# Performance work log

Hardware: AMD Instinct MI355X
Metric: run time of the kernel (lower is better)

The kernel has to match this reference:

```python
import jax, jax.numpy as jnp
import numpy as np
from math import sqrt

D_MODEL = 1024
B, T = 4, 4096


def setup_inputs() -> dict:
    key = jax.random.key(0)
    kx, kqk, kvo = jax.random.split(key, 3)
    x = jax.random.normal(kx, (B, T, D_MODEL), dtype=jnp.float32)
    # xavier_uniform for square [D, D]: limit = sqrt(6 / (D + D))
    limit = sqrt(6.0 / (2 * D_MODEL))
    QK = jax.random.uniform(kqk, (D_MODEL, D_MODEL), minval=-limit, maxval=limit, dtype=jnp.float32)
    VO = jax.random.uniform(kvo, (D_MODEL, D_MODEL), minval=-limit, maxval=limit, dtype=jnp.float32)
    return {"x": x, "QK": QK, "VO": VO}


def reference(x, QK, VO):
    d_model = QK.shape[0]
    # scores[b,t,u] = x[b,t,:] @ QK @ x[b,u,:]  -- precompute xQK once
    xQK = jnp.einsum('btd,de->bte', x, QK)                 # [B,T,D]
    scores = jnp.einsum('bte,bue->btu', xQK, x) / sqrt(d_model)  # [B,T,T]
    attn = jax.nn.softmax(scores, axis=2)
    # out[b,t,e] = attn @ x @ VO
    av = jnp.einsum('btu,bud->btd', attn, x)               # [B,T,D]
    return jnp.einsum('btd,de->bte', av, VO)
```

## Files before the change

### kernel.cpp

```cpp
#include <hip/hip_runtime.h>
#include <hip/hip_bf16.h>


#define BB 4
#define TT 4096
#define DD 1024

typedef __attribute__((ext_vector_type(8))) short bf16x8;
typedef __attribute__((ext_vector_type(4))) float f32x4;

__device__ __forceinline__ void gll16(const void* g, void* l) {
  __builtin_amdgcn_global_load_lds(
      (__attribute__((address_space(1))) void*)g,
      (__attribute__((address_space(3))) void*)l, 16, 0, 0);
}

#define WAIT_VM(n) asm volatile("s_waitcnt vmcnt(" #n ")" ::: "memory")
#define WAIT_LGKM0 do { asm volatile("s_waitcnt lgkmcnt(0)" ::: "memory"); \
                        __builtin_amdgcn_sched_barrier(0); } while (0)
#define BARRIER    do { __builtin_amdgcn_s_barrier(); \
                        __builtin_amdgcn_sched_barrier(0); } while (0)

__global__ __launch_bounds__(256) void xprep_k(const float* __restrict__ in,
                                               __hip_bfloat16* __restrict__ rm,
                                               __hip_bfloat16* __restrict__ cm,
                                               int R, int C, long bs) {
  in += (long)blockIdx.z * bs; rm += (long)blockIdx.z * bs; cm += (long)blockIdx.z * bs;
  __shared__ __hip_bfloat16 tile[64][65];
  int c0 = blockIdx.x * 64, r0 = blockIdx.y * 64;
  int tx = threadIdx.x & 63, ty = threadIdx.x >> 6;
#pragma unroll
  for (int i = 0; i < 16; ++i) {
    int r = ty + i * 4;
    __hip_bfloat16 v = __float2bfloat16(in[(long)(r0 + r) * C + c0 + tx]);
    tile[r][tx] = v;
    rm[(long)(r0 + r) * C + c0 + tx] = v;
  }
  __syncthreads();
#pragma unroll
  for (int i = 0; i < 16; ++i) {
    int c = ty + i * 4;
    cm[(long)(c0 + c) * R + r0 + tx] = tile[tx][c];
  }
}

__global__ __launch_bounds__(256) void transpose_cast_k(const float* __restrict__ in,
                                                        __hip_bfloat16* __restrict__ out,
                                                        int R, int C) {
  __shared__ __hip_bfloat16 tile[64][65];
  int c0 = blockIdx.x * 64, r0 = blockIdx.y * 64;
  int tx = threadIdx.x & 63, ty = threadIdx.x >> 6;
#pragma unroll
  for (int i = 0; i < 16; ++i) {
    int r = ty + i * 4;
    tile[r][tx] = __float2bfloat16(in[(long)(r0 + r) * C + c0 + tx]);
  }
  __syncthreads();
#pragma unroll
  for (int i = 0; i < 16; ++i) {
    int c = ty + i * 4;
    out[(long)(c0 + c) * R + r0 + tx] = tile[tx][c];
  }
}

__global__ __launch_bounds__(256) void zero_f32_k(float* __restrict__ p, int n) {
  int i = blockIdx.x * 256 + threadIdx.x;
  if (i < n) p[i] = 0.f;
}

template <typename OUT_T, int EPI>
__global__ __launch_bounds__(512, 2) void gemm256(
    const __hip_bfloat16* __restrict__ A,
    const __hip_bfloat16* __restrict__ Bt,
    OUT_T* __restrict__ C,
    int M, int N, int K, float alpha,
    long sAz, long sBz, long sCz, float* __restrict__ lsum) {
  __shared__ alignas(16) char smem[131072];
  A  += (long)blockIdx.z * sAz;
  Bt += (long)blockIdx.z * sBz;
  C  += (long)blockIdx.z * sCz;

  const int nwg = gridDim.x * gridDim.y;
  const int lin = blockIdx.x + gridDim.x * blockIdx.y;
  const int swz = (lin & 7) * (nwg >> 3) + (lin >> 3);
  const int gxsh = __popc(gridDim.x - 1);
  const int bx = swz & (gridDim.x - 1);
  const int by = swz >> gxsh;

  const int tid  = threadIdx.x;
  const int lane = tid & 63;
  const int wid  = tid >> 6;
  const int wr   = wid >> 2;
  const int wc   = wid & 3;
  const long m0 = (long)bx * 256;
  const long n0 = (long)by * 256;
  const int NT = K >> 6;

  const int srow = tid >> 3;
  const int sswz = (tid & 7) ^ (srow & 7);
  const __hip_bfloat16* gA = A  + (m0 + srow) * (long)K + sswz * 8;
  const __hip_bfloat16* gB = Bt + (n0 + srow) * (long)K + sswz * 8;

#define STG_A(s, c, D) gll16(gA + (long)(c) * 64 * K + (long)(s) * 64, \
                             smem + (D) + (c) * 8192 + wid * 1024)
#define STG_B(s, c, D) gll16(gB + (long)(c) * 64 * K + (long)(s) * 64, \
                             smem + (D) + 32768 + (c) * 8192 + wid * 1024)

  const int fr = lane & 15, l4 = lane >> 4, f7 = lane & 7;
  const char* a00 = smem +         (wr * 128 + fr) * 128 + ((l4    ) ^ f7) * 16;
  const char* a01 = smem +         (wr * 128 + fr) * 128 + ((4 | l4) ^ f7) * 16;
  const char* b00 = smem + 32768 + (wc * 64  + fr) * 128 + ((l4    ) ^ f7) * 16;
  const char* b01 = smem + 32768 + (wc * 64  + fr) * 128 + ((4 | l4) ^ f7) * 16;
  const char* a10 = a00 + 65536; const char* a11 = a01 + 65536;
  const char* b10 = b00 + 65536; const char* b11 = b01 + 65536;

  bf16x8 aq[4][2], bq[4][2];
#define RD_A(p0, p1, MIOFF)                                         \
  _Pragma("unroll") for (int mi_ = 0; mi_ < 4; ++mi_) {             \
    aq[mi_][0] = *(const bf16x8*)((p0) + ((MIOFF) + mi_) * 2048);   \
    aq[mi_][1] = *(const bf16x8*)((p1) + ((MIOFF) + mi_) * 2048);   \
  }
#define RD_B(p0, p1, NI0)                                           \
  _Pragma("unroll") for (int ni_ = 0; ni_ < 2; ++ni_) {             \
    bq[(NI0) + ni_][0] = *(const bf16x8*)((p0) + ((NI0) + ni_) * 2048); \
    bq[(NI0) + ni_][1] = *(const bf16x8*)((p1) + ((NI0) + ni_) * 2048); \
  }

  f32x4 acc[8][4];
#pragma unroll
  for (int mi = 0; mi < 8; ++mi)
#pragma unroll
    for (int ni = 0; ni < 4; ++ni)
      acc[mi][ni] = (f32x4){0.f, 0.f, 0.f, 0.f};

#define MFMA16(MI0, NI0)                                                       \
  do {                                                                         \
    __builtin_amdgcn_s_setprio(1);                                             \
    _Pragma("unroll") for (int ks_ = 0; ks_ < 2; ++ks_)                        \
    _Pragma("unroll") for (int mi_ = 0; mi_ < 4; ++mi_)                        \
    _Pragma("unroll") for (int ni_ = 0; ni_ < 2; ++ni_)                        \
      acc[(MI0) + mi_][(NI0) + ni_] = __builtin_amdgcn_mfma_f32_16x16x32_bf16( \
          aq[mi_][ks_], bq[(NI0) + ni_][ks_], acc[(MI0) + mi_][(NI0) + ni_],   \
          0, 0, 0);                                                            \
    __builtin_amdgcn_s_setprio(0);                                             \
  } while (0)

#pragma unroll
  for (int c = 0; c < 4; ++c) STG_A(0, c, 0);
#pragma unroll
  for (int c = 0; c < 4; ++c) STG_B(0, c, 0);
#pragma unroll
  for (int c = 0; c < 4; ++c) STG_A(1, c, 65536);
#pragma unroll
  for (int c = 0; c < 4; ++c) STG_B(1, c, 65536);
  WAIT_VM(8);
  BARRIER;

  for (int t2 = 0; t2 < NT; t2 += 2) {
    const bool g = (t2 + 2 < NT);
    RD_A(a00, a01, 0); RD_B(b00, b01, 0);
    asm volatile("s_waitcnt lgkmcnt(8)");
    BARRIER; WAIT_LGKM0; MFMA16(0, 0); BARRIER;
    RD_B(b00, b01, 2);
    BARRIER; WAIT_LGKM0; MFMA16(0, 2); BARRIER;
    RD_A(a00, a01, 4);
    if (g) { STG_B(t2 + 2, 0, 0); STG_B(t2 + 2, 1, 0);
             STG_B(t2 + 2, 2, 0); STG_B(t2 + 2, 3, 0); }
    BARRIER; WAIT_LGKM0; MFMA16(4, 2); BARRIER;
    if (g) { STG_A(t2 + 2, 0, 0); STG_A(t2 + 2, 1, 0);
             STG_A(t2 + 2, 2, 0); STG_A(t2 + 2, 3, 0); }
    MFMA16(4, 0);
    if (g) { WAIT_VM(8); } else { WAIT_VM(0); }
    BARRIER;
    RD_A(a10, a11, 0); RD_B(b10, b11, 0);
    asm volatile("s_waitcnt lgkmcnt(8)");
    BARRIER; WAIT_LGKM0; MFMA16(0, 0); BARRIER;
    RD_B(b10, b11, 2);
    BARRIER; WAIT_LGKM0; MFMA16(0, 2); BARRIER;
    RD_A(a10, a11, 4);
    if (g) { STG_B(t2 + 3, 0, 65536); STG_B(t2 + 3, 1, 65536);
             STG_B(t2 + 3, 2, 65536); STG_B(t2 + 3, 3, 65536); }
    BARRIER; WAIT_LGKM0; MFMA16(4, 2); BARRIER;
    if (g) { STG_A(t2 + 3, 0, 65536); STG_A(t2 + 3, 1, 65536);
             STG_A(t2 + 3, 2, 65536); STG_A(t2 + 3, 3, 65536); }
    MFMA16(4, 0);
    if (g) { WAIT_VM(8); } else { WAIT_VM(0); }
    BARRIER;
  }

  if constexpr (EPI == 2) {
    float* lred = (float*)smem;
    __syncthreads();
    for (int i = tid; i < 1024; i += 512) lred[i] = 0.f;
    __syncthreads();
#pragma unroll
    for (int mi = 0; mi < 8; ++mi) {
#pragma unroll
      for (int r = 0; r < 4; ++r) {
        const int rloc = wr * 128 + mi * 16 + (l4 << 2) + r;
        const long row = m0 + rloc;
        float rs = 0.f;
#pragma unroll
        for (int ni = 0; ni < 4; ++ni) {
          float e = __expf(acc[mi][ni][r] * alpha);
          long col = n0 + wc * 64 + ni * 16 + fr;
          C[row * (long)N + col] = (OUT_T)__float2bfloat16(e);
          rs += e;
        }
        rs += __shfl_xor(rs, 1); rs += __shfl_xor(rs, 2);
        rs += __shfl_xor(rs, 4); rs += __shfl_xor(rs, 8);
        if (fr == 0) lred[rloc * 4 + wc] = rs;
      }
    }
    __syncthreads();
    if (tid < 256) {
      float s4 = lred[tid * 4] + lred[tid * 4 + 1] + lred[tid * 4 + 2] + lred[tid * 4 + 3];
      atomicAdd(&lsum[(long)blockIdx.z * M + m0 + tid], s4);
    }
  } else if constexpr (EPI == 3) {
#pragma unroll
    for (int mi = 0; mi < 8; ++mi) {
      const long row = m0 + wr * 128 + mi * 16 + (l4 << 2);
      float4 lv = *(const float4*)&lsum[(long)blockIdx.z * M + row];
      float inv[4] = {1.f / lv.x, 1.f / lv.y, 1.f / lv.z, 1.f / lv.w};
#pragma unroll
      for (int ni = 0; ni < 4; ++ni) {
        long col = n0 + wc * 64 + ni * 16 + fr;
#pragma unroll
        for (int r = 0; r < 4; ++r)
          C[(row + r) * (long)N + col] = (OUT_T)__float2bfloat16(acc[mi][ni][r] * inv[r]);
      }
    }
  } else {
#pragma unroll
    for (int mi = 0; mi < 8; ++mi)
#pragma unroll
      for (int ni = 0; ni < 4; ++ni)
#pragma unroll
        for (int r = 0; r < 4; ++r) {
          long row = m0 + wr * 128 + mi * 16 + (l4 << 2) + r;
          long col = n0 + wc * 64 + ni * 16 + fr;
          float v = acc[mi][ni][r] * alpha;
          if constexpr (EPI == 0)
            C[row * (long)N + col] = v;
          else
            C[row * (long)N + col] = (OUT_T)__float2bfloat16(v);
        }
  }
#undef STG_A
#undef STG_B
#undef RD_A
#undef RD_B
#undef MFMA16
}

extern "C" void kernel_launch(void* const* d_in, const int* in_sizes, int n_in,
                              void* d_out, int out_size, void* d_ws, size_t ws_size,
                              hipStream_t stream) {
  const float* x  = (const float*)d_in[0];
  const float* QK = (const float*)d_in[1];
  const float* VO = (const float*)d_in[2];
  char* ws = (char*)d_ws;

  const long MB = 1l << 20;
  __hip_bfloat16* QKT  = (__hip_bfloat16*)(ws);
  float*          lsum = (float*)(ws);
  __hip_bfloat16* VOT  = (__hip_bfloat16*)(ws + 2 * MB);
  __hip_bfloat16* xb   = (__hip_bfloat16*)(ws + 4 * MB);
  __hip_bfloat16* xT   = (__hip_bfloat16*)(ws + 36 * MB);
  __hip_bfloat16* attn = (__hip_bfloat16*)(ws + 68 * MB);
  __hip_bfloat16* xqk  = (__hip_bfloat16*)d_out;

  const long NTOK = (long)BB * TT;
  const long bstride = (long)TT * DD;
  const long aslot = (long)TT * TT;

  xprep_k<<<dim3(DD / 64, TT / 64, BB), 256, 0, stream>>>(x, xb, xT, TT, DD, bstride);
  transpose_cast_k<<<dim3(16, 16, 1), 256, 0, stream>>>(QK, QKT, DD, DD);
  transpose_cast_k<<<dim3(16, 16, 1), 256, 0, stream>>>(VO, VOT, DD, DD);

  gemm256<__hip_bfloat16, 1><<<dim3(TT / 256, DD / 256, BB), 512, 0, stream>>>(
      xb, QKT, xqk, TT, DD, DD, 1.0f, bstride, 0, bstride, nullptr);

  zero_f32_k<<<(int)(NTOK / 256), 256, 0, stream>>>(lsum, (int)NTOK);

  gemm256<__hip_bfloat16, 2><<<dim3(TT / 256, TT / 256, BB), 512, 0, stream>>>(
      xqk, xb, attn, TT, TT, DD, 0.03125f, bstride, bstride, aslot, lsum);

  gemm256<__hip_bfloat16, 3><<<dim3(TT / 256, DD / 256, BB), 512, 0, stream>>>(
      attn, xT, xb, TT, DD, TT, 1.0f, aslot, bstride, bstride, lsum);

  gemm256<float, 0><<<dim3((int)(NTOK / 256), DD / 256, 1), 512, 0, stream>>>(
      xb, VOT, (float*)d_out, (int)NTOK, DD, DD, 1.0f, 0, 0, 0, nullptr);
}
```

Baseline: 369.3 us.

## Switch GEMM core to 32x32x16 MFMA with simplified double-buffered loop

Replaces the 16x16x32 bf16 MFMA tiles with 32x32x16 MFMA tiles, so each wave holds 4x2 blocks of 16-float accumulators. The main loop is restructured from a finely interleaved two-stage schedule with many barriers into a simpler per-k-tile loop: load all fragments from LDS, barrier, issue the next global-to-LDS prefetch, then run all MFMAs. The larger MFMA shape cuts instruction count and LDS reads per FLOP. The trade-off is less overlap between LDS reads and MFMAs, and epilogues are rewritten for the new accumulator layout, including staging inverse row sums in LDS.

```diff
diff --git a/kernel.cpp b/kernel.cpp
--- a/kernel.cpp
+++ b/kernel.cpp
@@ -7,7 +7,7 @@
 #define DD 1024
 
 typedef __attribute__((ext_vector_type(8))) short bf16x8;
-typedef __attribute__((ext_vector_type(4))) float f32x4;
+typedef __attribute__((ext_vector_type(16))) float f32x16;
 
 __device__ __forceinline__ void gll16(const void* g, void* l) {
   __builtin_amdgcn_global_load_lds(
@@ -106,44 +106,21 @@
 #define STG_B(s, c, D) gll16(gB + (long)(c) * 64 * K + (long)(s) * 64, \
                              smem + (D) + 32768 + (c) * 8192 + wid * 1024)
 
-  const int fr = lane & 15, l4 = lane >> 4, f7 = lane & 7;
-  const char* a00 = smem +         (wr * 128 + fr) * 128 + ((l4    ) ^ f7) * 16;
-  const char* a01 = smem +         (wr * 128 + fr) * 128 + ((4 | l4) ^ f7) * 16;
-  const char* b00 = smem + 32768 + (wc * 64  + fr) * 128 + ((l4    ) ^ f7) * 16;
-  const char* b01 = smem + 32768 + (wc * 64  + fr) * 128 + ((4 | l4) ^ f7) * 16;
-  const char* a10 = a00 + 65536; const char* a11 = a01 + 65536;
-  const char* b10 = b00 + 65536; const char* b11 = b01 + 65536;
-
-  bf16x8 aq[4][2], bq[4][2];
-#define RD_A(p0, p1, MIOFF)                                         \
-  _Pragma("unroll") for (int mi_ = 0; mi_ < 4; ++mi_) {             \
-    aq[mi_][0] = *(const bf16x8*)((p0) + ((MIOFF) + mi_) * 2048);   \
-    aq[mi_][1] = *(const bf16x8*)((p1) + ((MIOFF) + mi_) * 2048);   \
-  }
-#define RD_B(p0, p1, NI0)                                           \
-  _Pragma("unroll") for (int ni_ = 0; ni_ < 2; ++ni_) {             \
-    bq[(NI0) + ni_][0] = *(const bf16x8*)((p0) + ((NI0) + ni_) * 2048); \
-    bq[(NI0) + ni_][1] = *(const bf16x8*)((p1) + ((NI0) + ni_) * 2048); \
-  }
-
-  f32x4 acc[8][4];
-#pragma unroll
-  for (int mi = 0; mi < 8; ++mi)
-#pragma unroll
-    for (int ni = 0; ni < 4; ++ni)
-      acc[mi][ni] = (f32x4){0.f, 0.f, 0.f, 0.f};
-
-#define MFMA16(MI0, NI0)                                                       \
-  do {                                                                         \
-    __builtin_amdgcn_s_setprio(1);                                             \
-    _Pragma("unroll") for (int ks_ = 0; ks_ < 2; ++ks_)                        \
-    _Pragma("unroll") for (int mi_ = 0; mi_ < 4; ++mi_)                        \
-    _Pragma("unroll") for (int ni_ = 0; ni_ < 2; ++ni_)                        \
-      acc[(MI0) + mi_][(NI0) + ni_] = __builtin_amdgcn_mfma_f32_16x16x32_bf16( \
-          aq[mi_][ks_], bq[(NI0) + ni_][ks_], acc[(MI0) + mi_][(NI0) + ni_],   \
-          0, 0, 0);                                                            \
-    __builtin_amdgcn_s_setprio(0);                                             \
-  } while (0)
+  const int h   = lane >> 5;
+  const int r32 = lane & 31;
+  const int r7  = r32 & 7;
+  int soff[4];
+#pragma unroll
+  for (int ks = 0; ks < 4; ++ks) soff[ks] = (((ks * 2 + h) ^ r7) << 4);
+  const int aoff = (wr * 128 + r32) * 128;
+  const int boff = 32768 + (wc * 64 + r32) * 128;
+
+  f32x16 acc[4][2];
+#pragma unroll
+  for (int mi = 0; mi < 4; ++mi)
+#pragma unroll
+    for (int ni = 0; ni < 2; ++ni)
+      acc[mi][ni] = (f32x16)(0.f);
 
 #pragma unroll
   for (int c = 0; c < 4; ++c) STG_A(0, c, 0);
@@ -154,62 +131,65 @@
 #pragma unroll
   for (int c = 0; c < 4; ++c) STG_B(1, c, 65536);
   WAIT_VM(8);
-  BARRIER;
-
-  for (int t2 = 0; t2 < NT; t2 += 2) {
-    const bool g = (t2 + 2 < NT);
-    RD_A(a00, a01, 0); RD_B(b00, b01, 0);
-    asm volatile("s_waitcnt lgkmcnt(8)");
-    BARRIER; WAIT_LGKM0; MFMA16(0, 0); BARRIER;
-    RD_B(b00, b01, 2);
-    BARRIER; WAIT_LGKM0; MFMA16(0, 2); BARRIER;
-    RD_A(a00, a01, 4);
-    if (g) { STG_B(t2 + 2, 0, 0); STG_B(t2 + 2, 1, 0);
-             STG_B(t2 + 2, 2, 0); STG_B(t2 + 2, 3, 0); }
-    BARRIER; WAIT_LGKM0; MFMA16(4, 2); BARRIER;
-    if (g) { STG_A(t2 + 2, 0, 0); STG_A(t2 + 2, 1, 0);
-             STG_A(t2 + 2, 2, 0); STG_A(t2 + 2, 3, 0); }
-    MFMA16(4, 0);
-    if (g) { WAIT_VM(8); } else { WAIT_VM(0); }
+
+  for (int t = 0; t < NT; ++t) {
     BARRIER;
-    RD_A(a10, a11, 0); RD_B(b10, b11, 0);
-    asm volatile("s_waitcnt lgkmcnt(8)");
-    BARRIER; WAIT_LGKM0; MFMA16(0, 0); BARRIER;
-    RD_B(b10, b11, 2);
-    BARRIER; WAIT_LGKM0; MFMA16(0, 2); BARRIER;
-    RD_A(a10, a11, 4);
-    if (g) { STG_B(t2 + 3, 0, 65536); STG_B(t2 + 3, 1, 65536);
-             STG_B(t2 + 3, 2, 65536); STG_B(t2 + 3, 3, 65536); }
-    BARRIER; WAIT_LGKM0; MFMA16(4, 2); BARRIER;
-    if (g) { STG_A(t2 + 3, 0, 65536); STG_A(t2 + 3, 1, 65536);
-             STG_A(t2 + 3, 2, 65536); STG_A(t2 + 3, 3, 65536); }
-    MFMA16(4, 0);
-    if (g) { WAIT_VM(8); } else { WAIT_VM(0); }
+    const char* bs = smem + (t & 1) * 65536;
+    bf16x8 aq[4][4], bq[2][4];
+#pragma unroll
+    for (int mi = 0; mi < 4; ++mi)
+#pragma unroll
+      for (int ks = 0; ks < 4; ++ks)
+        aq[mi][ks] = *(const bf16x8*)(bs + aoff + mi * 4096 + soff[ks]);
+#pragma unroll
+    for (int ni = 0; ni < 2; ++ni)
+#pragma unroll
+      for (int ks = 0; ks < 4; ++ks)
+        bq[ni][ks] = *(const bf16x8*)(bs + boff + ni * 4096 + soff[ks]);
+    WAIT_LGKM0;
     BARRIER;
-  }
-
+    if (t + 2 < NT) {
+      const int D_ = (t & 1) * 65536;
+      STG_B(t + 2, 0, D_); STG_B(t + 2, 1, D_);
+      STG_B(t + 2, 2, D_); STG_B(t + 2, 3, D_);
+      STG_A(t + 2, 0, D_); STG_A(t + 2, 1, D_);
+      STG_A(t + 2, 2, D_); STG_A(t + 2, 3, D_);
+    }
+    __builtin_amdgcn_s_setprio(1);
+#pragma unroll
+    for (int ks = 0; ks < 4; ++ks)
+#pragma unroll
+      for (int mi = 0; mi < 4; ++mi)
+#pragma unroll
+        for (int ni = 0; ni < 2; ++ni)
+          acc[mi][ni] = __builtin_amdgcn_mfma_f32_32x32x16_bf16(
+              aq[mi][ks], bq[ni][ks], acc[mi][ni], 0, 0, 0);
+    __builtin_amdgcn_s_setprio(0);
+    if (t + 2 < NT)      { WAIT_VM(8); }
+    else if (t + 1 < NT) { WAIT_VM(0); }
+  }
+
+  const long colb = n0 + wc * 64 + r32;
   if constexpr (EPI == 2) {
     float* lred = (float*)smem;
     __syncthreads();
-    for (int i = tid; i < 1024; i += 512) lred[i] = 0.f;
-    __syncthreads();
-#pragma unroll
-    for (int mi = 0; mi < 8; ++mi) {
-#pragma unroll
-      for (int r = 0; r < 4; ++r) {
-        const int rloc = wr * 128 + mi * 16 + (l4 << 2) + r;
+#pragma unroll
+    for (int mi = 0; mi < 4; ++mi) {
+#pragma unroll
+      for (int reg = 0; reg < 16; ++reg) {
+        const int rloc = wr * 128 + mi * 32 + (reg & 3) + 8 * (reg >> 2) + 4 * h;
         const long row = m0 + rloc;
         float rs = 0.f;
 #pragma unroll
-        for (int ni = 0; ni < 4; ++ni) {
-          float e = __expf(acc[mi][ni][r] * alpha);
-          long col = n0 + wc * 64 + ni * 16 + fr;
-          C[row * (long)N + col] = (OUT_T)__float2bfloat16(e);
+        for (int ni = 0; ni < 2; ++ni) {
+          float e = __expf(acc[mi][ni][reg] * alpha);
+          C[row * (long)N + colb + ni * 32] = (OUT_T)__float2bfloat16(e);
           rs += e;
         }
-        rs += __shfl_xor(rs, 1); rs += __shfl_xor(rs, 2);
-        rs += __shfl_xor(rs, 4); rs += __shfl_xor(rs, 8);
-        if (fr == 0) lred[rloc * 4 + wc] = rs;
+        rs += __shfl_xor(rs, 1);  rs += __shfl_xor(rs, 2);
+        rs += __shfl_xor(rs, 4);  rs += __shfl_xor(rs, 8);
+        rs += __shfl_xor(rs, 16);
+        if (r32 == 0) lred[rloc * 4 + wc] = rs;
       }
     }
     __syncthreads();
@@ -218,40 +198,41 @@
       atomicAdd(&lsum[(long)blockIdx.z * M + m0 + tid], s4);
     }
   } else if constexpr (EPI == 3) {
-#pragma unroll
-    for (int mi = 0; mi < 8; ++mi) {
-      const long row = m0 + wr * 128 + mi * 16 + (l4 << 2);
-      float4 lv = *(const float4*)&lsum[(long)blockIdx.z * M + row];
-      float inv[4] = {1.f / lv.x, 1.f / lv.y, 1.f / lv.z, 1.f / lv.w};
-#pragma unroll
-      for (int ni = 0; ni < 4; ++ni) {
-        long col = n0 + wc * 64 + ni * 16 + fr;
-#pragma unroll
-        for (int r = 0; r < 4; ++r)
-          C[(row + r) * (long)N + col] = (OUT_T)__float2bfloat16(acc[mi][ni][r] * inv[r]);
+    float* linv = (float*)smem;
+    __syncthreads();
+    if (tid < 256) linv[tid] = 1.0f / lsum[(long)blockIdx.z * M + m0 + tid];
+    __syncthreads();
+#pragma unroll
+    for (int mi = 0; mi < 4; ++mi) {
+#pragma unroll
+      for (int reg = 0; reg < 16; ++reg) {
+        const int rloc = wr * 128 + mi * 32 + (reg & 3) + 8 * (reg >> 2) + 4 * h;
+        const float inv = linv[rloc];
+        const long row = m0 + rloc;
+#pragma unroll
+        for (int ni = 0; ni < 2; ++ni)
+          C[row * (long)N + colb + ni * 32] =
+              (OUT_T)__float2bfloat16(acc[mi][ni][reg] * inv);
       }
     }
   } else {
 #pragma unroll
-    for (int mi = 0; mi < 8; ++mi)
-#pragma unroll
-      for (int ni = 0; ni < 4; ++ni)
-#pragma unroll
-        for (int r = 0; r < 4; ++r) {
-          long row = m0 + wr * 128 + mi * 16 + (l4 << 2) + r;
-          long col = n0 + wc * 64 + ni * 16 + fr;
-          float v = acc[mi][ni][r] * alpha;
+    for (int mi = 0; mi < 4; ++mi)
+#pragma unroll
+      for (int reg = 0; reg < 16; ++reg) {
+        const long row = m0 + wr * 128 + mi * 32 + (reg & 3) + 8 * (reg >> 2) + 4 * h;
+#pragma unroll
+        for (int ni = 0; ni < 2; ++ni) {
+          float v = acc[mi][ni][reg] * alpha;
           if constexpr (EPI == 0)
-            C[row * (long)N + col] = v;
+            C[row * (long)N + colb + ni * 32] = v;
           else
-            C[row * (long)N + col] = (OUT_T)__float2bfloat16(v);
+            C[row * (long)N + colb + ni * 32] = (OUT_T)__float2bfloat16(v);
         }
+      }
   }
 #undef STG_A
 #undef STG_B
-#undef RD_A
-#undef RD_B
-#undef MFMA16
 }
 
 extern "C" void kernel_launch(void* const* d_in, const int* in_sizes, int n_in,
```

After: 479.4 us. 1.3x slower.
